# Kernel tuning notes

Hardware: AMD Instinct MI355X
Metric: run time of the kernel (lower is better)

Reference implementation:

```python
import jax, jax.numpy as jnp
import numpy as np

# PLN channel layout per 51-channel group:
#   0      : existence prob
#   1:21   : 20 class probs
#   21:23  : xy offsets (unused in get_poss)
#   23:37  : x-link probs (14)
#   37:51  : y-link probs (14)

def _get_poss(cor, cen):
    # cor, cen: [N, 51, 14, 14]  (spatial index i = ix*14+iy)
    # out[n,c,ix,iy,sx,sy] = 0.5 * cor0[n,ix,iy]*cen0[n,sx,sy]
    #   * corC[n,c,ix,iy]*cenC[n,c,sx,sy]
    #   * cor[n,23+sx,ix,iy]*cor[n,37+sy,ix,iy]
    #   * cen[n,23+ix,sx,sy]*cen[n,37+iy,sx,sy]
    A = (cor[:, 0:1] * cor[:, 1:21])[:, :, :, :, None, None]          # [N,20,ix,iy,1,1]
    B = (cen[:, 0:1] * cen[:, 1:21])[:, :, None, None, :, :]          # [N,20,1,1,sx,sy]
    Lcx = jnp.transpose(cor[:, 23:37], (0, 2, 3, 1))[:, None, :, :, :, None]  # [N,1,ix,iy,sx,1]
    Lcy = jnp.transpose(cor[:, 37:51], (0, 2, 3, 1))[:, None, :, :, None, :]  # [N,1,ix,iy,1,sy]
    Lsx = cen[:, 23:37][:, None, :, None, :, :]                       # [N,1,ix,1,sx,sy]
    Lsy = cen[:, 37:51][:, None, None, :, :, :]                       # [N,1,1,iy,sx,sy]
    return 0.5 * A * B * Lcx * Lcy * Lsx * Lsy                        # [N,20,14,14,14,14]


def setup_inputs() -> dict:
    key = jax.random.key(0)
    inference = jax.random.uniform(key, (32, 204, 14, 14), dtype=jnp.float32)
    return {"inference": inference}


def reference(inference):
    N = inference.shape[0]
    g = inference.reshape(N, 4, 51, 14, 14)
    corner1, corner2, center1, center2 = g[:, 0], g[:, 1], g[:, 2], g[:, 3]
    p1 = _get_poss(corner1, center1)
    p2 = _get_poss(corner2, center1)
    p3 = _get_poss(corner1, center2)
    p4 = _get_poss(corner2, center2)
    return (p1, p2, p3, p4)
```

## Files before the change

### kernel.cpp

```cpp
#include <hip/hip_runtime.h>


#define S_PER 24586240u
#define TSTRIDE (51 * 196)
#define N_STRIDE (204 * 196)

__global__ __launch_bounds__(256) void plnet_kernel(const float* __restrict__ in,
                                                    float* __restrict__ out) {
    __shared__ __align__(16) float sT1[196];
    __shared__ __align__(16) float sT2[196];
    __shared__ float sA1[196], sA2[196];
    __shared__ float sB1[196], sB2[196];

    const unsigned b  = blockIdx.x;
    const unsigned d2 = b % 14u;
    const unsigned nq = b / 14u;
    const unsigned q  = nq % 20u;
    const unsigned n  = nq / 20u;

    const float* g    = in + (size_t)n * N_STRIDE;
    const float* cor1 = g;
    const float* cor2 = g + TSTRIDE;
    const float* cen1 = g + 2 * TSTRIDE;
    const float* cen2 = g + 3 * TSTRIDE;

    const unsigned tid = threadIdx.x;

    if (tid < 196u) {
        const unsigned ps = tid;
        sT1[ps] = cen1[ps] * cen1[(1u + q) * 196u + ps] * cen1[(23u + d2) * 196u + ps];
        sT2[ps] = cen2[ps] * cen2[(1u + q) * 196u + ps] * cen2[(23u + d2) * 196u + ps];
        const unsigned d3 = ps / 14u;
        const unsigned k  = ps - d3 * 14u;
        const unsigned pc = d2 * 14u + d3;
        const float k1 = 0.5f * cor1[pc] * cor1[(1u + q) * 196u + pc];
        const float k2 = 0.5f * cor2[pc] * cor2[(1u + q) * 196u + pc];
        sA1[ps] = k1 * cor1[(23u + k) * 196u + pc];
        sA2[ps] = k2 * cor2[(23u + k) * 196u + pc];
        sB1[ps] = cor1[(37u + k) * 196u + pc];
        sB2[ps] = cor2[(37u + k) * 196u + pc];
    }
    __syncthreads();

    const size_t chunk = ((size_t)(n * 20u + q) * 196u + d2 * 14u) * 196u;
    float4* o1 = (float4*)(out + chunk);
    float4* o2 = (float4*)(out + (size_t)S_PER + chunk);
    float4* o3 = (float4*)(out + 2u * (size_t)S_PER + chunk);
    float4* o4 = (float4*)(out + 3u * (size_t)S_PER + chunk);

    for (unsigned c = tid; c < 686u; c += 256u) {
        const unsigned d3 = c / 49u;
        const unsigned f  = c - d3 * 49u;
        const unsigned e  = 4u * f;

        const float4 t1 = *(const float4*)&sT1[e];
        const float4 t2 = *(const float4*)&sT2[e];
        const float4 v1 = *(const float4*)&cen1[(37u + d3) * 196u + e];
        const float4 v2 = *(const float4*)&cen2[(37u + d3) * 196u + e];

        const float4 G1 = make_float4(t1.x * v1.x, t1.y * v1.y, t1.z * v1.z, t1.w * v1.w);
        const float4 G2 = make_float4(t2.x * v2.x, t2.y * v2.y, t2.z * v2.z, t2.w * v2.w);

        unsigned d4 = e / 14u;
        unsigned d5 = e - d4 * 14u;
        float F1[4], F2[4];
#pragma unroll
        for (int l = 0; l < 4; ++l) {
            F1[l] = sA1[d3 * 14u + d4] * sB1[d3 * 14u + d5];
            F2[l] = sA2[d3 * 14u + d4] * sB2[d3 * 14u + d5];
            ++d5;
            const unsigned carry = (d5 == 14u);
            d4 += carry;
            d5 = carry ? 0u : d5;
        }

        o1[c] = make_float4(F1[0] * G1.x, F1[1] * G1.y, F1[2] * G1.z, F1[3] * G1.w);
        o2[c] = make_float4(F2[0] * G1.x, F2[1] * G1.y, F2[2] * G1.z, F2[3] * G1.w);
        o3[c] = make_float4(F1[0] * G2.x, F1[1] * G2.y, F1[2] * G2.z, F1[3] * G2.w);
        o4[c] = make_float4(F2[0] * G2.x, F2[1] * G2.y, F2[2] * G2.z, F2[3] * G2.w);
    }
}

extern "C" void kernel_launch(void* const* d_in, const int* in_sizes, int n_in,
                              void* d_out, int out_size, void* d_ws, size_t ws_size,
                              hipStream_t stream) {
    const float* in = (const float*)d_in[0];
    float* out = (float*)d_out;
    dim3 grid(32 * 20 * 14);
    dim3 block(256);
    plnet_kernel<<<grid, block, 0, stream>>>(in, out);
}
```

Measured before the change: 89.52 us.

## Process four classes per block, reusing class-independent factors across them

Each block now covers four class indices instead of one. The class-independent corner link products and center link products are computed once into shared memory and reused for every class, and the grid shrinks by four. This is meant to cut redundant setup loads and arithmetic per output element. In exchange it uses more shared memory and registers and launches fewer blocks, which could reduce occupancy in a kernel that is mostly bound by store bandwidth.

```diff
diff --git a/kernel.cpp b/kernel.cpp
--- a/kernel.cpp
+++ b/kernel.cpp
@@ -7,16 +7,17 @@
 
 __global__ __launch_bounds__(256) void plnet_kernel(const float* __restrict__ in,
                                                     float* __restrict__ out) {
-    __shared__ __align__(16) float sT1[196];
-    __shared__ __align__(16) float sT2[196];
-    __shared__ float sA1[196], sA2[196];
-    __shared__ float sB1[196], sB2[196];
+    __shared__ __align__(16) float sFc1[2744];
+    __shared__ __align__(16) float sFc2[2744];
+    __shared__ __align__(16) float sU1[196], sU2[196];
+    __shared__ float sA1[196], sA2[196], sB1[196], sB2[196];
+    __shared__ float sKq1[56], sKq2[56];
 
     const unsigned b  = blockIdx.x;
-    const unsigned d2 = b % 14u;
-    const unsigned nq = b / 14u;
-    const unsigned q  = nq % 20u;
-    const unsigned n  = nq / 20u;
+    const unsigned qg = b % 5u;
+    const unsigned r0 = b / 5u;
+    const unsigned d2 = r0 % 14u;
+    const unsigned n  = r0 / 14u;
 
     const float* g    = in + (size_t)n * N_STRIDE;
     const float* cor1 = g;
@@ -28,56 +29,106 @@
 
     if (tid < 196u) {
         const unsigned ps = tid;
-        sT1[ps] = cen1[ps] * cen1[(1u + q) * 196u + ps] * cen1[(23u + d2) * 196u + ps];
-        sT2[ps] = cen2[ps] * cen2[(1u + q) * 196u + ps] * cen2[(23u + d2) * 196u + ps];
+        sU1[ps] = cen1[ps] * cen1[(23u + d2) * 196u + ps];
+        sU2[ps] = cen2[ps] * cen2[(23u + d2) * 196u + ps];
         const unsigned d3 = ps / 14u;
         const unsigned k  = ps - d3 * 14u;
         const unsigned pc = d2 * 14u + d3;
-        const float k1 = 0.5f * cor1[pc] * cor1[(1u + q) * 196u + pc];
-        const float k2 = 0.5f * cor2[pc] * cor2[(1u + q) * 196u + pc];
-        sA1[ps] = k1 * cor1[(23u + k) * 196u + pc];
-        sA2[ps] = k2 * cor2[(23u + k) * 196u + pc];
+        sA1[ps] = 0.5f * cor1[pc] * cor1[(23u + k) * 196u + pc];
+        sA2[ps] = 0.5f * cor2[pc] * cor2[(23u + k) * 196u + pc];
         sB1[ps] = cor1[(37u + k) * 196u + pc];
         sB2[ps] = cor2[(37u + k) * 196u + pc];
     }
+    if (tid < 112u) {
+        const unsigned j  = tid / 28u;
+        const unsigned r  = tid - 28u * j;
+        const unsigned i  = r / 14u;
+        const unsigned d3 = r - 14u * i;
+        const unsigned q  = qg + 5u * j;
+        const unsigned pc = d2 * 14u + d3;
+        if (i == 0u) sKq1[j * 14u + d3] = cor1[(1u + q) * 196u + pc];
+        else         sKq2[j * 14u + d3] = cor2[(1u + q) * 196u + pc];
+    }
     __syncthreads();
-
-    const size_t chunk = ((size_t)(n * 20u + q) * 196u + d2 * 14u) * 196u;
-    float4* o1 = (float4*)(out + chunk);
-    float4* o2 = (float4*)(out + (size_t)S_PER + chunk);
-    float4* o3 = (float4*)(out + 2u * (size_t)S_PER + chunk);
-    float4* o4 = (float4*)(out + 3u * (size_t)S_PER + chunk);
 
     for (unsigned c = tid; c < 686u; c += 256u) {
         const unsigned d3 = c / 49u;
-        const unsigned f  = c - d3 * 49u;
+        const unsigned f  = c - 49u * d3;
         const unsigned e  = 4u * f;
-
-        const float4 t1 = *(const float4*)&sT1[e];
-        const float4 t2 = *(const float4*)&sT2[e];
-        const float4 v1 = *(const float4*)&cen1[(37u + d3) * 196u + e];
-        const float4 v2 = *(const float4*)&cen2[(37u + d3) * 196u + e];
-
-        const float4 G1 = make_float4(t1.x * v1.x, t1.y * v1.y, t1.z * v1.z, t1.w * v1.w);
-        const float4 G2 = make_float4(t2.x * v2.x, t2.y * v2.y, t2.z * v2.z, t2.w * v2.w);
-
         unsigned d4 = e / 14u;
-        unsigned d5 = e - d4 * 14u;
-        float F1[4], F2[4];
+        unsigned d5 = e - 14u * d4;
+        float f1[4], f2[4];
 #pragma unroll
         for (int l = 0; l < 4; ++l) {
-            F1[l] = sA1[d3 * 14u + d4] * sB1[d3 * 14u + d5];
-            F2[l] = sA2[d3 * 14u + d4] * sB2[d3 * 14u + d5];
+            f1[l] = sA1[d3 * 14u + d4] * sB1[d3 * 14u + d5];
+            f2[l] = sA2[d3 * 14u + d4] * sB2[d3 * 14u + d5];
             ++d5;
             const unsigned carry = (d5 == 14u);
             d4 += carry;
             d5 = carry ? 0u : d5;
         }
+        ((float4*)sFc1)[c] = make_float4(f1[0], f1[1], f1[2], f1[3]);
+        ((float4*)sFc2)[c] = make_float4(f2[0], f2[1], f2[2], f2[3]);
+    }
+    __syncthreads();
 
-        o1[c] = make_float4(F1[0] * G1.x, F1[1] * G1.y, F1[2] * G1.z, F1[3] * G1.w);
-        o2[c] = make_float4(F2[0] * G1.x, F2[1] * G1.y, F2[2] * G1.z, F2[3] * G1.w);
-        o3[c] = make_float4(F1[0] * G2.x, F1[1] * G2.y, F1[2] * G2.z, F1[3] * G2.w);
-        o4[c] = make_float4(F2[0] * G2.x, F2[1] * G2.y, F2[2] * G2.z, F2[3] * G2.w);
+    float4 u1h[3], u2h[3], fc1h[3], fc2h[3], v1h[3], v2h[3];
+    unsigned d3h[3], eh[3];
+#pragma unroll
+    for (int k = 0; k < 3; ++k) {
+        const unsigned c  = tid + 256u * (unsigned)k;
+        const unsigned cc = (c < 686u) ? c : 0u;
+        const unsigned d3 = cc / 49u;
+        const unsigned f  = cc - 49u * d3;
+        const unsigned e  = 4u * f;
+        d3h[k] = d3; eh[k] = e;
+        u1h[k]  = *(const float4*)&sU1[e];
+        u2h[k]  = *(const float4*)&sU2[e];
+        fc1h[k] = ((const float4*)sFc1)[cc];
+        fc2h[k] = ((const float4*)sFc2)[cc];
+        v1h[k]  = *(const float4*)&cen1[(37u + d3) * 196u + e];
+        v2h[k]  = *(const float4*)&cen2[(37u + d3) * 196u + e];
+    }
+
+#pragma unroll
+    for (unsigned j = 0; j < 4u; ++j) {
+        const unsigned q = qg + 5u * j;
+        const size_t chunk = ((size_t)(n * 20u + q) * 196u + d2 * 14u) * 196u;
+        float4* o1 = (float4*)(out + chunk);
+        float4* o2 = (float4*)(out + (size_t)S_PER + chunk);
+        float4* o3 = (float4*)(out + 2u * (size_t)S_PER + chunk);
+        float4* o4 = (float4*)(out + 3u * (size_t)S_PER + chunk);
+        const float* xr1 = &cen1[(1u + q) * 196u];
+        const float* xr2 = &cen2[(1u + q) * 196u];
+
+#pragma unroll
+        for (int k = 0; k < 3; ++k) {
+            const unsigned c = tid + 256u * (unsigned)k;
+            if (c < 686u) {
+                const float4 x1 = *(const float4*)&xr1[eh[k]];
+                const float4 x2 = *(const float4*)&xr2[eh[k]];
+                const float kq1 = sKq1[j * 14u + d3h[k]];
+                const float kq2 = sKq2[j * 14u + d3h[k]];
+
+                const float4 g1 = make_float4(u1h[k].x * x1.x * v1h[k].x,
+                                              u1h[k].y * x1.y * v1h[k].y,
+                                              u1h[k].z * x1.z * v1h[k].z,
+                                              u1h[k].w * x1.w * v1h[k].w);
+                const float4 g2 = make_float4(u2h[k].x * x2.x * v2h[k].x,
+                                              u2h[k].y * x2.y * v2h[k].y,
+                                              u2h[k].z * x2.z * v2h[k].z,
+                                              u2h[k].w * x2.w * v2h[k].w);
+                const float4 h1 = make_float4(fc1h[k].x * kq1, fc1h[k].y * kq1,
+                                              fc1h[k].z * kq1, fc1h[k].w * kq1);
+                const float4 h2 = make_float4(fc2h[k].x * kq2, fc2h[k].y * kq2,
+                                              fc2h[k].z * kq2, fc2h[k].w * kq2);
+
+                o1[c] = make_float4(h1.x * g1.x, h1.y * g1.y, h1.z * g1.z, h1.w * g1.w);
+                o2[c] = make_float4(h2.x * g1.x, h2.y * g1.y, h2.z * g1.z, h2.w * g1.w);
+                o3[c] = make_float4(h1.x * g2.x, h1.y * g2.y, h1.z * g2.z, h1.w * g2.w);
+                o4[c] = make_float4(h2.x * g2.x, h2.y * g2.y, h2.z * g2.z, h2.w * g2.w);
+            }
+        }
     }
 }
 
@@ -86,7 +137,7 @@
                               hipStream_t stream) {
     const float* in = (const float*)d_in[0];
     float* out = (float*)d_out;
-    dim3 grid(32 * 20 * 14);
+    dim3 grid(32 * 14 * 5);
     dim3 block(256);
     plnet_kernel<<<grid, block, 0, stream>>>(in, out);
 }
```

New measurement: 93.63 us. 1.05x slower.
